# Performance work log

Hardware: AMD Instinct MI355X
Metric: run time of the kernel (lower is better)

The kernel has to match this reference:

```python
import jax, jax.numpy as jnp
import numpy as np

D_MODEL = 1024
NUM_HEADS = 16
WINDOW = 128
DEPTH = D_MODEL // NUM_HEADS


def setup_inputs() -> dict:
    key = jax.random.key(0)
    ks = jax.random.split(key, 9)
    B, S = 2, 2048
    scale = 1.0 / np.sqrt(D_MODEL)
    x = jax.random.normal(ks[0], (B, S, D_MODEL), dtype=jnp.float32)
    Wq = jax.random.normal(ks[1], (D_MODEL, D_MODEL), dtype=jnp.float32) * scale
    Wk = jax.random.normal(ks[2], (D_MODEL, D_MODEL), dtype=jnp.float32) * scale
    Wv = jax.random.normal(ks[3], (D_MODEL, D_MODEL), dtype=jnp.float32) * scale
    Wo = jax.random.normal(ks[4], (D_MODEL, D_MODEL), dtype=jnp.float32) * scale
    bq = jnp.zeros((D_MODEL,), jnp.float32)
    bk = jnp.zeros((D_MODEL,), jnp.float32)
    bv = jnp.zeros((D_MODEL,), jnp.float32)
    bo = jnp.zeros((D_MODEL,), jnp.float32)
    return {"x": x, "Wq": Wq, "bq": bq, "Wk": Wk, "bk": bk,
            "Wv": Wv, "bv": bv, "Wo": Wo, "bo": bo}


def _split_heads(t, B, S):
    # [B,S,D] -> [B,H,S,depth]
    return t.reshape(B, S, NUM_HEADS, DEPTH).transpose(0, 2, 1, 3)


def reference(x, Wq, bq, Wk, bk, Wv, bv, Wo, bo):
    B, S, _ = x.shape
    q = _split_heads(x @ Wq + bq, B, S)
    k = _split_heads(x @ Wk + bk, B, S)
    v = _split_heads(x @ Wv + bv, B, S)
    scores = jnp.einsum('bhqd,bhkd->bhqk', q, k) / jnp.sqrt(jnp.float32(DEPTH))
    idx = jnp.arange(S)
    # mask[i_row=j, i_col=i] per original: |i - j| <= window (symmetric)
    local = jnp.abs(idx[None, :] - idx[:, None]) <= WINDOW  # [S,S]
    scores = jnp.where(local[None, None], scores, jnp.float32(-1e9))
    attn = jax.nn.softmax(scores, axis=-1)
    out = jnp.einsum('bhqk,bhkd->bhqd', attn, v)
    concat = out.transpose(0, 2, 1, 3).reshape(B, S, D_MODEL)
    return concat @ Wo + bo
```

## Files before the change

kernel.cpp:

```cpp
#include <hip/hip_runtime.h>
#include <cstdint>
#include <cstddef>

typedef __attribute__((ext_vector_type(8))) short short8;
typedef __attribute__((ext_vector_type(4))) short short4v;
typedef __attribute__((ext_vector_type(4))) float f32x4;
typedef short8 bf16x8;

typedef __attribute__((address_space(1))) const unsigned GU;
typedef __attribute__((address_space(3))) unsigned LU;

__device__ __forceinline__ short f2bf(float f) {
  unsigned u = __builtin_bit_cast(unsigned, f);
  u += 0x7fffu + ((u >> 16) & 1u);
  return (short)(u >> 16);
}

__global__ __launch_bounds__(256) void k_cast_x(const float* __restrict__ x, short* __restrict__ xb) {
  size_t i = ((size_t)blockIdx.x * 256 + threadIdx.x) * 8;
  f32x4 a = *(const f32x4*)(x + i);
  f32x4 b = *(const f32x4*)(x + i + 4);
  short8 o;
#pragma unroll
  for (int j = 0; j < 4; ++j) { o[j] = f2bf(a[j]); o[4 + j] = f2bf(b[j]); }
  *(short8*)(xb + i) = o;
}

__global__ __launch_bounds__(256) void k_tw(const float* __restrict__ W0, const float* __restrict__ W1,
                                            const float* __restrict__ W2, const float* __restrict__ W3,
                                            short* __restrict__ WT) {
  __shared__ short T[64 * 72];
  int bid = blockIdx.x;
  int widx = bid >> 8;
  int t = bid & 255;
  int kr = (t >> 4) * 64, nc = (t & 15) * 64;
  const float* W = widx == 0 ? W0 : widx == 1 ? W1 : widx == 2 ? W2 : W3;
  short* out = WT + (size_t)widx * 1048576;
  int tid = threadIdx.x;
#pragma unroll
  for (int i = 0; i < 4; ++i) {
    int idx = tid + i * 256;
    int k = idx >> 4, n4 = (idx & 15) << 2;
    f32x4 v = *(const f32x4*)(W + (size_t)(kr + k) * 1024 + nc + n4);
#pragma unroll
    for (int j = 0; j < 4; ++j) T[(n4 + j) * 72 + k] = f2bf(v[j]);
  }
  __syncthreads();
#pragma unroll
  for (int i = 0; i < 2; ++i) {
    int idx = tid + i * 256;
    int n = idx >> 3, k8 = (idx & 7) << 3;
    *(short8*)(out + (size_t)(nc + n) * 1024 + kr + k8) = *(const short8*)&T[n * 72 + k8];
  }
}

__global__ __launch_bounds__(256) void k_tv(const short* __restrict__ v, short* __restrict__ vT) {
  __shared__ short T[64 * 72];
  int bid = blockIdx.x;
  int stile = bid & 31, h = (bid >> 5) & 15, b = bid >> 9;
  int s0 = stile * 64;
  int tid = threadIdx.x;
#pragma unroll
  for (int i = 0; i < 2; ++i) {
    int idx = tid + i * 256;
    int s = idx >> 3, d0 = (idx & 7) << 3;
    short8 vec = *(const short8*)(v + ((size_t)b * 2048 + s0 + s) * 1024 + h * 64 + d0);
#pragma unroll
    for (int j = 0; j < 8; ++j) T[(d0 + j) * 72 + s] = vec[j];
  }
  __syncthreads();
#pragma unroll
  for (int i = 0; i < 2; ++i) {
    int idx = tid + i * 256;
    int d = idx >> 3, s8 = (idx & 7) << 3;
    *(short8*)(vT + (((size_t)b * 16 + h) * 64 + d) * 2048 + s0 + s8) = *(const short8*)&T[d * 72 + s8];
  }
}

__global__ __launch_bounds__(512, 2) void k_gemm256(
    const short* __restrict__ A, const short* __restrict__ BT,
    const float* __restrict__ bias0, const float* __restrict__ bias1, const float* __restrict__ bias2,
    short* __restrict__ outb) {
  __shared__ short S[65536];
  const int tid = threadIdx.x;
  const int lane = tid & 63, w = tid >> 6;
  const int g = lane >> 4, qi = lane & 15;
  const int wm = w >> 2, wn = w & 3;
  int bid = blockIdx.x;
  int swz = (bid & 7) * 24 + (bid >> 3);
  const int tm = swz / 12, tn = swz % 12;
  const int m0 = tm * 256, n0 = tn * 256;
  const size_t K = 1024;
  const short* Ab = A + (size_t)m0 * K;
  const short* Bb = BT + (size_t)n0 * K;

  auto stage = [&](int roff, const short* gbase, int kt, int kh) {
    int k0 = kt * 64 + kh * 32;
#pragma unroll
    for (int i = 0; i < 2; ++i) {
      int c = tid + i * 512;
      int r = c >> 2;
      int csw = ((c & 3) ^ ((r >> 1) & 3)) << 3;
      __builtin_amdgcn_global_load_lds((GU*)(gbase + (size_t)r * K + k0 + csw),
                                       (LU*)(&S[roff + c * 8]), 16, 0, 0);
    }
  };
  auto lda = [&](int roff, int row) -> bf16x8 {
    return *(const bf16x8*)&S[roff + row * 32 + ((g ^ ((row >> 1) & 3)) << 3)];
  };

  f32x4 acc[8][4];
#pragma unroll
  for (int i = 0; i < 8; ++i)
#pragma unroll
    for (int j = 0; j < 4; ++j) acc[i][j] = (f32x4)(0.0f);

#define MF1(rh, mf, nf, av, bv) \
  acc[(rh)*4+(mf)][(nf)] = __builtin_amdgcn_mfma_f32_16x16x32_bf16(av, bv, acc[(rh)*4+(mf)][(nf)], 0, 0, 0)

#define GPH(buf, kh, rh, ...) do { \
    const int ra_ = (buf)*32768 + (kh)*8192; \
    const int rb_ = (buf)*32768 + 16384 + (kh)*8192; \
    const int ar_ = wm*128 + (rh)*64 + qi; \
    bf16x8 a0 = lda(ra_, ar_ + 0);  bf16x8 a1 = lda(ra_, ar_ + 16); \
    bf16x8 a2 = lda(ra_, ar_ + 32); bf16x8 a3 = lda(ra_, ar_ + 48); \
    const int br_ = wn*64 + qi; \
    bf16x8 b0 = lda(rb_, br_ + 0);  bf16x8 b1 = lda(rb_, br_ + 16); \
    bf16x8 b2 = lda(rb_, br_ + 32); bf16x8 b3 = lda(rb_, br_ + 48); \
    __VA_ARGS__; \
    __builtin_amdgcn_sched_barrier(0); \
    __builtin_amdgcn_s_barrier(); \
    asm volatile("s_waitcnt lgkmcnt(0)" ::: "memory"); \
    __builtin_amdgcn_sched_barrier(0); \
    __builtin_amdgcn_s_setprio(1); \
    MF1(rh,0,0,a0,b0); MF1(rh,0,1,a0,b1); MF1(rh,0,2,a0,b2); MF1(rh,0,3,a0,b3); \
    MF1(rh,1,0,a1,b0); MF1(rh,1,1,a1,b1); MF1(rh,1,2,a1,b2); MF1(rh,1,3,a1,b3); \
    MF1(rh,2,0,a2,b0); MF1(rh,2,1,a2,b1); MF1(rh,2,2,a2,b2); MF1(rh,2,3,a2,b3); \
    MF1(rh,3,0,a3,b0); MF1(rh,3,1,a3,b1); MF1(rh,3,2,a3,b2); MF1(rh,3,3,a3,b3); \
    __builtin_amdgcn_s_setprio(0); \
    __builtin_amdgcn_sched_barrier(0); \
  } while (0)

  stage(0,     Ab, 0, 0);
  stage(16384, Bb, 0, 0);
  stage(8192,  Ab, 0, 1);
  stage(24576, Bb, 0, 1);
  stage(32768, Ab, 1, 0);
  stage(49152, Bb, 1, 0);
  asm volatile("s_waitcnt vmcnt(4)" ::: "memory");
  __builtin_amdgcn_s_barrier();

  for (int j = 0; j < 8; ++j) {
    int t1 = 2 * j + 1;
    int t2 = 2 * j + 2; t2 = t2 < 15 ? t2 : 15;
    int t3 = 2 * j + 3; t3 = t3 < 15 ? t3 : 15;
    GPH(0, 0, 0, stage(40960, Ab, t1, 1));  __builtin_amdgcn_s_barrier();
    GPH(0, 0, 1, stage(57344, Bb, t1, 1));  __builtin_amdgcn_s_barrier();
    GPH(0, 1, 0, stage(0,     Ab, t2, 0));  __builtin_amdgcn_s_barrier();
    GPH(0, 1, 1, stage(16384, Bb, t2, 0));
      asm volatile("s_waitcnt vmcnt(4)" ::: "memory");
      __builtin_amdgcn_s_barrier();
    GPH(1, 0, 0, stage(8192,  Ab, t2, 1));  __builtin_amdgcn_s_barrier();
    GPH(1, 0, 1, stage(24576, Bb, t2, 1));  __builtin_amdgcn_s_barrier();
    GPH(1, 1, 0, stage(32768, Ab, t3, 0));  __builtin_amdgcn_s_barrier();
    GPH(1, 1, 1, stage(49152, Bb, t3, 0));
      asm volatile("s_waitcnt vmcnt(4)" ::: "memory");
      __builtin_amdgcn_s_barrier();
  }
#undef GPH
#undef MF1

  asm volatile("s_waitcnt vmcnt(0)" ::: "memory");
  __syncthreads();
  int sel = n0 >> 10;
  const float* bias = sel == 0 ? bias0 : (sel == 1 ? bias1 : bias2);
  size_t outoff = (size_t)sel * 4194304;
  int ncol0 = n0 & 1023;
  float bv[4];
#pragma unroll
  for (int nf = 0; nf < 4; ++nf) bv[nf] = bias[ncol0 + wn * 64 + nf * 16 + qi];
  short* Ep = S;
#pragma unroll
  for (int rh = 0; rh < 2; ++rh) {
    __syncthreads();
#pragma unroll
    for (int mf = 0; mf < 4; ++mf)
#pragma unroll
      for (int nf = 0; nf < 4; ++nf)
#pragma unroll
        for (int j = 0; j < 4; ++j)
          Ep[(wm * 64 + mf * 16 + g * 4 + j) * 264 + wn * 64 + nf * 16 + qi] =
              f2bf(acc[rh * 4 + mf][nf][j] + bv[nf]);
    __syncthreads();
#pragma unroll
    for (int i = 0; i < 8; ++i) {
      int idx = tid + i * 512;
      int r = idx >> 5, c8 = (idx & 31) << 3;
      int grow = m0 + (r >> 6) * 128 + rh * 64 + (r & 63);
      *(short8*)&outb[outoff + (size_t)grow * 1024 + ncol0 + c8] = *(const short8*)&Ep[r * 264 + c8];
    }
  }
}

__global__ __launch_bounds__(256, 2) void k_gemmO(
    const short* __restrict__ A, const short* __restrict__ BT,
    const float* __restrict__ bias0, float* __restrict__ outf) {
  __shared__ short Smem[16384];
  const int tid = threadIdx.x;
  const int lane = tid & 63, w = tid >> 6;
  const int g = lane >> 4, qi = lane & 15;
  const int wr = (w >> 1) * 64, wc = (w & 1) * 64;
  const int m0 = blockIdx.y * 128, n0 = blockIdx.x * 128;
  const size_t K = 1024;
  const short* Ab = A + (size_t)m0 * K;
  const short* Bb = BT + (size_t)n0 * K;

  auto stage = [&](int buf, int k0) {
    short* Asb = Smem + buf * 4096;
    short* Bsb = Smem + 8192 + buf * 4096;
#pragma unroll
    for (int i = 0; i < 2; ++i) {
      int cidx = tid + i * 256;
      int r = cidx >> 2;
      int csw = ((cidx & 3) ^ ((r >> 1) & 3)) << 3;
      __builtin_amdgcn_global_load_lds((GU*)(Ab + (size_t)r * K + k0 + csw),
                                       (LU*)(&Asb[cidx * 8]), 16, 0, 0);
      __builtin_amdgcn_global_load_lds((GU*)(Bb + (size_t)r * K + k0 + csw),
                                       (LU*)(&Bsb[cidx * 8]), 16, 0, 0);
    }
  };

  f32x4 acc[4][4];
#pragma unroll
  for (int i = 0; i < 4; ++i)
#pragma unroll
    for (int j = 0; j < 4; ++j) acc[i][j] = (f32x4)(0.0f);

  stage(0, 0);
  __syncthreads();
  for (int kt = 0; kt < 32; ++kt) {
    int cur = kt & 1;
    if (kt < 31) stage(cur ^ 1, (kt + 1) * 32);
    const short* Asb = Smem + cur * 4096;
    const short* Bsb = Smem + 8192 + cur * 4096;
    bf16x8 a[4], b[4];
#pragma unroll
    for (int mf = 0; mf < 4; ++mf) {
      int R = wr + mf * 16 + qi;
      a[mf] = *(const bf16x8*)&Asb[R * 32 + ((g ^ ((R >> 1) & 3)) << 3)];
    }
#pragma unroll
    for (int nf = 0; nf < 4; ++nf) {
      int R = wc + nf * 16 + qi;
      b[nf] = *(const bf16x8*)&Bsb[R * 32 + ((g ^ ((R >> 1) & 3)) << 3)];
    }
#pragma unroll
    for (int mf = 0; mf < 4; ++mf)
#pragma unroll
      for (int nf = 0; nf < 4; ++nf)
        acc[mf][nf] = __builtin_amdgcn_mfma_f32_16x16x32_bf16(a[mf], b[nf], acc[mf][nf], 0, 0, 0);
    __syncthreads();
  }

  float* Ft = (float*)Smem;
  float bv[4];
#pragma unroll
  for (int nf = 0; nf < 4; ++nf) bv[nf] = bias0[n0 + wc + nf * 16 + qi];
#pragma unroll
  for (int mf = 0; mf < 4; ++mf) {
    __syncthreads();
#pragma unroll
    for (int nf = 0; nf < 4; ++nf)
#pragma unroll
      for (int j = 0; j < 4; ++j)
        Ft[((w >> 1) * 16 + g * 4 + j) * 136 + wc + nf * 16 + qi] = acc[mf][nf][j] + bv[nf];
    __syncthreads();
#pragma unroll
    for (int i = 0; i < 4; ++i) {
      int idx = tid + i * 256;
      int r = idx >> 5, c4 = (idx & 31) << 2;
      int row = m0 + ((r >> 4) << 6) + mf * 16 + (r & 15);
      *(f32x4*)&outf[(size_t)row * 1024 + n0 + c4] = *(const f32x4*)&Ft[r * 136 + c4];
    }
  }
}

__global__ __launch_bounds__(256, 2) void k_attn(const short* __restrict__ qg_,
                                                 const short* __restrict__ kg_,
                                                 const short* __restrict__ vT,
                                                 short* __restrict__ outp) {
  __shared__ short Qs[64 * 72];
  __shared__ short Ks[64 * 72];
  __shared__ short Vs[64 * 72];
  __shared__ short Ps[4][16 * 72];
  int bid = blockIdx.x;
  int qt = bid & 31, h = (bid >> 5) & 15, b = bid >> 9;
  int q0 = qt * 64;
  int tid = threadIdx.x, lane = tid & 63, w = tid >> 6;
  int g = lane >> 4, qi = lane & 15;

  const short* qsrc = qg_ + ((size_t)b * 2048 + q0) * 1024 + h * 64;
#pragma unroll
  for (int i = 0; i < 2; ++i) {
    int idx = tid + i * 256;
    int r = idx >> 3, c = (idx & 7) << 3;
    *(short8*)&Qs[r * 72 + c] = *(const short8*)&qsrc[(size_t)r * 1024 + c];
  }

  float m = -1e30f, l = 0.f;
  f32x4 oacc[4];
#pragma unroll
  for (int i = 0; i < 4; ++i) oacc[i] = (f32x4)(0.0f);
  int qglob = q0 + w * 16 + qi;

  for (int cc = 0; cc < 5; ++cc) {
    int kb0 = q0 - 128 + cc * 64;
    if (kb0 < 0 || kb0 >= 2048) continue;
    __syncthreads();
    const short* ksrc = kg_ + ((size_t)b * 2048 + kb0) * 1024 + h * 64;
    const short* vsrc = vT + ((size_t)(b * 16 + h)) * 64 * 2048 + kb0;
#pragma unroll
    for (int i = 0; i < 2; ++i) {
      int idx = tid + i * 256;
      int r = idx >> 3, c = (idx & 7) << 3;
      *(short8*)&Ks[r * 72 + c] = *(const short8*)&ksrc[(size_t)r * 1024 + c];
      *(short8*)&Vs[r * 72 + c] = *(const short8*)&vsrc[(size_t)r * 2048 + c];
    }
    __syncthreads();

    f32x4 st[4];
#pragma unroll
    for (int i = 0; i < 4; ++i) st[i] = (f32x4)(0.0f);
#pragma unroll
    for (int ds = 0; ds < 2; ++ds) {
      bf16x8 qf = *(const bf16x8*)&Qs[(w * 16 + qi) * 72 + ds * 32 + g * 8];
#pragma unroll
      for (int mf = 0; mf < 4; ++mf) {
        bf16x8 kf = *(const bf16x8*)&Ks[(mf * 16 + qi) * 72 + ds * 32 + g * 8];
        st[mf] = __builtin_amdgcn_mfma_f32_16x16x32_bf16(kf, qf, st[mf], 0, 0, 0);
      }
    }

    float pv[16];
    float pm = -1e30f;
#pragma unroll
    for (int mf = 0; mf < 4; ++mf)
#pragma unroll
      for (int j = 0; j < 4; ++j) {
        int kcol = kb0 + mf * 16 + g * 4 + j;
        float s = st[mf][j] * 0.125f;
        int d = kcol - qglob;
        bool valid = (d >= -128) && (d <= 128);
        s = valid ? s : -1e30f;
        pv[mf * 4 + j] = s;
        pm = fmaxf(pm, s);
      }
    pm = fmaxf(pm, __shfl_xor(pm, 16));
    pm = fmaxf(pm, __shfl_xor(pm, 32));
    float mnew = fmaxf(m, pm);
    float scale = __expf(m - mnew);
    float ls = 0.f;
#pragma unroll
    for (int e = 0; e < 16; ++e) {
      float p = pv[e] > -1e29f ? __expf(pv[e] - mnew) : 0.f;
      pv[e] = p;
      ls += p;
    }
    ls += __shfl_xor(ls, 16);
    ls += __shfl_xor(ls, 32);
    l = l * scale + ls;
    m = mnew;
#pragma unroll
    for (int mf = 0; mf < 4; ++mf) oacc[mf] *= scale;

#pragma unroll
    for (int f = 0; f < 4; ++f) {
      short4v pk;
#pragma unroll
      for (int j = 0; j < 4; ++j) pk[j] = f2bf(pv[f * 4 + j]);
      *(short4v*)&Ps[w][qi * 72 + f * 16 + g * 4] = pk;
    }

#pragma unroll
    for (int ks = 0; ks < 2; ++ks) {
      bf16x8 pf = *(const bf16x8*)&Ps[w][qi * 72 + ks * 32 + g * 8];
#pragma unroll
      for (int mf = 0; mf < 4; ++mf) {
        bf16x8 vf = *(const bf16x8*)&Vs[(mf * 16 + qi) * 72 + ks * 32 + g * 8];
        oacc[mf] = __builtin_amdgcn_mfma_f32_16x16x32_bf16(vf, pf, oacc[mf], 0, 0, 0);
      }
    }
  }

  __syncthreads();
  short* Os = Ks;
  float inv = 1.f / l;
#pragma unroll
  for (int mf = 0; mf < 4; ++mf) {
    short4v pk;
#pragma unroll
    for (int j = 0; j < 4; ++j) pk[j] = f2bf(oacc[mf][j] * inv);
    *(short4v*)&Os[(w * 16 + qi) * 72 + mf * 16 + g * 4] = pk;
  }
  __syncthreads();
  short* dst = outp + ((size_t)b * 2048 + q0) * 1024 + h * 64;
  int r = tid >> 2, c16 = (tid & 3) << 4;
  *(short8*)&dst[(size_t)r * 1024 + c16] = *(const short8*)&Os[r * 72 + c16];
  *(short8*)&dst[(size_t)r * 1024 + c16 + 8] = *(const short8*)&Os[r * 72 + c16 + 8];
}

extern "C" void kernel_launch(void* const* d_in, const int* in_sizes, int n_in,
                              void* d_out, int out_size, void* d_ws, size_t ws_size,
                              hipStream_t stream) {
  const float* x  = (const float*)d_in[0];
  const float* Wq = (const float*)d_in[1];
  const float* bq = (const float*)d_in[2];
  const float* Wk = (const float*)d_in[3];
  const float* bk = (const float*)d_in[4];
  const float* Wv = (const float*)d_in[5];
  const float* bv = (const float*)d_in[6];
  const float* Wo = (const float*)d_in[7];
  const float* bo = (const float*)d_in[8];

  short* ws = (short*)d_ws;
  short* xb       = ws;
  short* qkv      = ws + 4194304;
  short* vbuf     = qkv + 2 * 4194304;
  short* vT       = ws;
  short* attn_out = vbuf;
  short* WT       = ws + 4 * 4194304;

  k_cast_x<<<2048, 256, 0, stream>>>(x, xb);
  k_tw<<<1024, 256, 0, stream>>>(Wq, Wk, Wv, Wo, WT);
  k_gemm256<<<192, 512, 0, stream>>>(xb, WT, bq, bk, bv, qkv);
  k_tv<<<1024, 256, 0, stream>>>(vbuf, vT);
  k_attn<<<1024, 256, 0, stream>>>(qkv, qkv + 4194304, vT, attn_out);
  {
    dim3 grid(8, 32);
    k_gemmO<<<grid, 256, 0, stream>>>(attn_out, WT + 3 * 1048576, bo, (float*)d_out);
  }
}
```

Baseline: 92.98 us.

## Switch QKV GEMM from 16x16x32 to 32x32x16 MFMA tiles

Reworks the fused QKV projection GEMM so each wave computes its 128x64 tile with 32x32x16 bf16 MFMA instructions instead of 16x16x32. This cuts the number of LDS fragment loads per MFMA and restructures the per-phase schedule, with partial lgkmcnt waits so half the MFMAs can start while the rest of the LDS reads finish. The epilogue is rewritten for the 32x32 accumulator layout. Larger accumulators and a different LDS access pattern may change register pressure and bank conflicts.

```diff
diff --git a/kernel.cpp b/kernel.cpp
--- a/kernel.cpp
+++ b/kernel.cpp
@@ -5,6 +5,7 @@
 typedef __attribute__((ext_vector_type(8))) short short8;
 typedef __attribute__((ext_vector_type(4))) short short4v;
 typedef __attribute__((ext_vector_type(4))) float f32x4;
+typedef __attribute__((ext_vector_type(16))) float f32x16;
 typedef short8 bf16x8;
 
 typedef __attribute__((address_space(1))) const unsigned GU;
@@ -84,7 +85,7 @@
   __shared__ short S[65536];
   const int tid = threadIdx.x;
   const int lane = tid & 63, w = tid >> 6;
-  const int g = lane >> 4, qi = lane & 15;
+  const int l31 = lane & 31, hi = lane >> 5;
   const int wm = w >> 2, wn = w & 3;
   int bid = blockIdx.x;
   int swz = (bid & 7) * 24 + (bid >> 3);
@@ -105,38 +106,58 @@
                                        (LU*)(&S[roff + c * 8]), 16, 0, 0);
     }
   };
-  auto lda = [&](int roff, int row) -> bf16x8 {
-    return *(const bf16x8*)&S[roff + row * 32 + ((g ^ ((row >> 1) & 3)) << 3)];
+  auto lda = [&](int roff, int row, int s) -> bf16x8 {
+    int c = (s * 2 + hi) ^ ((row >> 1) & 3);
+    return *(const bf16x8*)&S[roff + row * 32 + c * 8];
   };
 
-  f32x4 acc[8][4];
-#pragma unroll
-  for (int i = 0; i < 8; ++i)
-#pragma unroll
-    for (int j = 0; j < 4; ++j) acc[i][j] = (f32x4)(0.0f);
-
-#define MF1(rh, mf, nf, av, bv) \
-  acc[(rh)*4+(mf)][(nf)] = __builtin_amdgcn_mfma_f32_16x16x32_bf16(av, bv, acc[(rh)*4+(mf)][(nf)], 0, 0, 0)
-
-#define GPH(buf, kh, rh, ...) do { \
-    const int ra_ = (buf)*32768 + (kh)*8192; \
-    const int rb_ = (buf)*32768 + 16384 + (kh)*8192; \
-    const int ar_ = wm*128 + (rh)*64 + qi; \
-    bf16x8 a0 = lda(ra_, ar_ + 0);  bf16x8 a1 = lda(ra_, ar_ + 16); \
-    bf16x8 a2 = lda(ra_, ar_ + 32); bf16x8 a3 = lda(ra_, ar_ + 48); \
-    const int br_ = wn*64 + qi; \
-    bf16x8 b0 = lda(rb_, br_ + 0);  bf16x8 b1 = lda(rb_, br_ + 16); \
-    bf16x8 b2 = lda(rb_, br_ + 32); bf16x8 b3 = lda(rb_, br_ + 48); \
-    __VA_ARGS__; \
+  f32x16 acc[4][2];
+#pragma unroll
+  for (int i = 0; i < 4; ++i)
+#pragma unroll
+    for (int j = 0; j < 2; ++j) acc[i][j] = (f32x16)(0.0f);
+
+#define MFA(mi, ni, av, bv) \
+  acc[mi][ni] = __builtin_amdgcn_mfma_f32_32x32x16_bf16(av, bv, acc[mi][ni], 0, 0, 0)
+#define VMC4 asm volatile("s_waitcnt vmcnt(4)" ::: "memory")
+#define NOVM (void)0
+
+#define GPP(buf, kh, STG0, STG1, VM1) do { \
+    const int rA_ = (buf)*32768 + (kh)*8192; \
+    const int rB_ = (buf)*32768 + 16384 + (kh)*8192; \
+    const int ar_ = wm*128 + l31; \
+    const int br_ = wn*64 + l31; \
+    bf16x8 a00 = lda(rA_, ar_,      0); bf16x8 a10 = lda(rA_, ar_ + 32, 0); \
+    bf16x8 b00 = lda(rB_, br_,      0); bf16x8 b10 = lda(rB_, br_ + 32, 0); \
+    bf16x8 a01 = lda(rA_, ar_,      1); bf16x8 a11 = lda(rA_, ar_ + 32, 1); \
+    bf16x8 b01 = lda(rB_, br_,      1); bf16x8 b11 = lda(rB_, br_ + 32, 1); \
+    STG0; \
     __builtin_amdgcn_sched_barrier(0); \
     __builtin_amdgcn_s_barrier(); \
+    asm volatile("s_waitcnt lgkmcnt(4)" ::: "memory"); \
+    __builtin_amdgcn_sched_barrier(0); \
+    __builtin_amdgcn_s_setprio(1); \
+    MFA(0,0,a00,b00); MFA(0,1,a00,b10); MFA(1,0,a10,b00); MFA(1,1,a10,b10); \
+    __builtin_amdgcn_sched_barrier(0); \
     asm volatile("s_waitcnt lgkmcnt(0)" ::: "memory"); \
     __builtin_amdgcn_sched_barrier(0); \
+    MFA(0,0,a01,b01); MFA(0,1,a01,b11); MFA(1,0,a11,b01); MFA(1,1,a11,b11); \
+    __builtin_amdgcn_s_setprio(0); \
+    __builtin_amdgcn_sched_barrier(0); \
+    bf16x8 c00 = lda(rA_, ar_ + 64, 0); bf16x8 c10 = lda(rA_, ar_ + 96, 0); \
+    bf16x8 c01 = lda(rA_, ar_ + 64, 1); bf16x8 c11 = lda(rA_, ar_ + 96, 1); \
+    STG1; \
+    VM1; \
+    __builtin_amdgcn_sched_barrier(0); \
+    __builtin_amdgcn_s_barrier(); \
+    asm volatile("s_waitcnt lgkmcnt(2)" ::: "memory"); \
+    __builtin_amdgcn_sched_barrier(0); \
     __builtin_amdgcn_s_setprio(1); \
-    MF1(rh,0,0,a0,b0); MF1(rh,0,1,a0,b1); MF1(rh,0,2,a0,b2); MF1(rh,0,3,a0,b3); \
-    MF1(rh,1,0,a1,b0); MF1(rh,1,1,a1,b1); MF1(rh,1,2,a1,b2); MF1(rh,1,3,a1,b3); \
-    MF1(rh,2,0,a2,b0); MF1(rh,2,1,a2,b1); MF1(rh,2,2,a2,b2); MF1(rh,2,3,a2,b3); \
-    MF1(rh,3,0,a3,b0); MF1(rh,3,1,a3,b1); MF1(rh,3,2,a3,b2); MF1(rh,3,3,a3,b3); \
+    MFA(2,0,c00,b00); MFA(2,1,c00,b10); MFA(3,0,c10,b00); MFA(3,1,c10,b10); \
+    __builtin_amdgcn_sched_barrier(0); \
+    asm volatile("s_waitcnt lgkmcnt(0)" ::: "memory"); \
+    __builtin_amdgcn_sched_barrier(0); \
+    MFA(2,0,c01,b01); MFA(2,1,c01,b11); MFA(3,0,c11,b01); MFA(3,1,c11,b11); \
     __builtin_amdgcn_s_setprio(0); \
     __builtin_amdgcn_sched_barrier(0); \
   } while (0)
@@ -154,21 +175,13 @@
     int t1 = 2 * j + 1;
     int t2 = 2 * j + 2; t2 = t2 < 15 ? t2 : 15;
     int t3 = 2 * j + 3; t3 = t3 < 15 ? t3 : 15;
-    GPH(0, 0, 0, stage(40960, Ab, t1, 1));  __builtin_amdgcn_s_barrier();
-    GPH(0, 0, 1, stage(57344, Bb, t1, 1));  __builtin_amdgcn_s_barrier();
-    GPH(0, 1, 0, stage(0,     Ab, t2, 0));  __builtin_amdgcn_s_barrier();
-    GPH(0, 1, 1, stage(16384, Bb, t2, 0));
-      asm volatile("s_waitcnt vmcnt(4)" ::: "memory");
-      __builtin_amdgcn_s_barrier();
-    GPH(1, 0, 0, stage(8192,  Ab, t2, 1));  __builtin_amdgcn_s_barrier();
-    GPH(1, 0, 1, stage(24576, Bb, t2, 1));  __builtin_amdgcn_s_barrier();
-    GPH(1, 1, 0, stage(32768, Ab, t3, 0));  __builtin_amdgcn_s_barrier();
-    GPH(1, 1, 1, stage(49152, Bb, t3, 0));
-      asm volatile("s_waitcnt vmcnt(4)" ::: "memory");
-      __builtin_amdgcn_s_barrier();
-  }
-#undef GPH
-#undef MF1
+    GPP(0, 0, stage(40960, Ab, t1, 1), stage(57344, Bb, t1, 1), NOVM);
+    GPP(0, 1, stage(0,     Ab, t2, 0), stage(16384, Bb, t2, 0), VMC4);
+    GPP(1, 0, stage(8192,  Ab, t2, 1), stage(24576, Bb, t2, 1), NOVM);
+    GPP(1, 1, stage(32768, Ab, t3, 0), stage(49152, Bb, t3, 0), VMC4);
+  }
+#undef GPP
+#undef MFA
 
   asm volatile("s_waitcnt vmcnt(0)" ::: "memory");
   __syncthreads();
@@ -176,27 +189,31 @@
   const float* bias = sel == 0 ? bias0 : (sel == 1 ? bias1 : bias2);
   size_t outoff = (size_t)sel * 4194304;
   int ncol0 = n0 & 1023;
-  float bv[4];
-#pragma unroll
-  for (int nf = 0; nf < 4; ++nf) bv[nf] = bias[ncol0 + wn * 64 + nf * 16 + qi];
+  float bv[2];
+#pragma unroll
+  for (int ni = 0; ni < 2; ++ni) bv[ni] = bias[ncol0 + wn * 64 + ni * 32 + l31];
   short* Ep = S;
 #pragma unroll
-  for (int rh = 0; rh < 2; ++rh) {
-    __syncthreads();
-#pragma unroll
-    for (int mf = 0; mf < 4; ++mf)
-#pragma unroll
-      for (int nf = 0; nf < 4; ++nf)
-#pragma unroll
-        for (int j = 0; j < 4; ++j)
-          Ep[(wm * 64 + mf * 16 + g * 4 + j) * 264 + wn * 64 + nf * 16 + qi] =
-              f2bf(acc[rh * 4 + mf][nf][j] + bv[nf]);
+  for (int p = 0; p < 2; ++p) {
+    __syncthreads();
+#pragma unroll
+    for (int mi2 = 0; mi2 < 2; ++mi2)
+#pragma unroll
+      for (int ni = 0; ni < 2; ++ni)
+#pragma unroll
+        for (int rq = 0; rq < 4; ++rq)
+#pragma unroll
+          for (int jj = 0; jj < 4; ++jj) {
+            int rif = jj + 4 * hi + 8 * rq;
+            Ep[(wm * 64 + mi2 * 32 + rif) * 264 + wn * 64 + ni * 32 + l31] =
+                f2bf(acc[p * 2 + mi2][ni][rq * 4 + jj] + bv[ni]);
+          }
     __syncthreads();
 #pragma unroll
     for (int i = 0; i < 8; ++i) {
       int idx = tid + i * 512;
       int r = idx >> 5, c8 = (idx & 31) << 3;
-      int grow = m0 + (r >> 6) * 128 + rh * 64 + (r & 63);
+      int grow = m0 + (r >> 6) * 128 + p * 64 + (r & 63);
       *(short8*)&outb[outoff + (size_t)grow * 1024 + ncol0 + c8] = *(const short8*)&Ep[r * 264 + c8];
     }
   }
```

Result: no change. 92.61 us (-0.4%).

## Restructure QKV GEMM main loop into full-K64 stages with interleaved LDS reads

Applied to the files above, without the earlier changes.

Reworks the 256x256 QKV projection GEMM so each pipeline stage loads a full 64-wide K slice per 128-row half, with a new 8-way XOR swizzle. The hand-scheduled loop interleaves partial lgkmcnt waits with MFMA groups and issues the next tiles' global-to-LDS loads between compute chunks. This is meant to cut barriers per K step and overlap LDS reads with MFMA work. Warps now own contiguous 128-row strips, so the epilogue is reorganised to write one strip per pass. The cost is higher register pressure from double-buffered fragments and a more fragile wait-count schedule.

```diff
diff --git a/kernel.cpp b/kernel.cpp
--- a/kernel.cpp
+++ b/kernel.cpp
@@ -94,19 +94,18 @@
   const short* Ab = A + (size_t)m0 * K;
   const short* Bb = BT + (size_t)n0 * K;
 
-  auto stage = [&](int roff, const short* gbase, int kt, int kh) {
-    int k0 = kt * 64 + kh * 32;
+  auto stage = [&](int roff, const short* gbase, int kt) {
 #pragma unroll
     for (int i = 0; i < 2; ++i) {
-      int c = tid + i * 512;
-      int r = c >> 2;
-      int csw = ((c & 3) ^ ((r >> 1) & 3)) << 3;
-      __builtin_amdgcn_global_load_lds((GU*)(gbase + (size_t)r * K + k0 + csw),
-                                       (LU*)(&S[roff + c * 8]), 16, 0, 0);
+      int cc = tid + i * 512;
+      int r = cc >> 3;
+      int js = ((cc & 7) ^ (r & 7)) << 3;
+      __builtin_amdgcn_global_load_lds((GU*)(gbase + (size_t)r * K + kt * 64 + js),
+                                       (LU*)(&S[roff + cc * 8]), 16, 0, 0);
     }
   };
-  auto lda = [&](int roff, int row) -> bf16x8 {
-    return *(const bf16x8*)&S[roff + row * 32 + ((g ^ ((row >> 1) & 3)) << 3)];
+  auto lda = [&](int roff, int row, int kk) -> bf16x8 {
+    return *(const bf16x8*)&S[roff + row * 64 + (((kk * 4 + g) ^ (row & 7)) << 3)];
   };
 
   f32x4 acc[8][4];
@@ -115,60 +114,88 @@
 #pragma unroll
     for (int j = 0; j < 4; ++j) acc[i][j] = (f32x4)(0.0f);
 
-#define MF1(rh, mf, nf, av, bv) \
-  acc[(rh)*4+(mf)][(nf)] = __builtin_amdgcn_mfma_f32_16x16x32_bf16(av, bv, acc[(rh)*4+(mf)][(nf)], 0, 0, 0)
-
-#define GPH(buf, kh, rh, ...) do { \
-    const int ra_ = (buf)*32768 + (kh)*8192; \
-    const int rb_ = (buf)*32768 + 16384 + (kh)*8192; \
-    const int ar_ = wm*128 + (rh)*64 + qi; \
-    bf16x8 a0 = lda(ra_, ar_ + 0);  bf16x8 a1 = lda(ra_, ar_ + 16); \
-    bf16x8 a2 = lda(ra_, ar_ + 32); bf16x8 a3 = lda(ra_, ar_ + 48); \
-    const int br_ = wn*64 + qi; \
-    bf16x8 b0 = lda(rb_, br_ + 0);  bf16x8 b1 = lda(rb_, br_ + 16); \
-    bf16x8 b2 = lda(rb_, br_ + 32); bf16x8 b3 = lda(rb_, br_ + 48); \
-    __VA_ARGS__; \
-    __builtin_amdgcn_sched_barrier(0); \
-    __builtin_amdgcn_s_barrier(); \
-    asm volatile("s_waitcnt lgkmcnt(0)" ::: "memory"); \
-    __builtin_amdgcn_sched_barrier(0); \
-    __builtin_amdgcn_s_setprio(1); \
-    MF1(rh,0,0,a0,b0); MF1(rh,0,1,a0,b1); MF1(rh,0,2,a0,b2); MF1(rh,0,3,a0,b3); \
-    MF1(rh,1,0,a1,b0); MF1(rh,1,1,a1,b1); MF1(rh,1,2,a1,b2); MF1(rh,1,3,a1,b3); \
-    MF1(rh,2,0,a2,b0); MF1(rh,2,1,a2,b1); MF1(rh,2,2,a2,b2); MF1(rh,2,3,a2,b3); \
-    MF1(rh,3,0,a3,b0); MF1(rh,3,1,a3,b1); MF1(rh,3,2,a3,b2); MF1(rh,3,3,a3,b3); \
-    __builtin_amdgcn_s_setprio(0); \
-    __builtin_amdgcn_sched_barrier(0); \
-  } while (0)
-
-  stage(0,     Ab, 0, 0);
-  stage(16384, Bb, 0, 0);
-  stage(8192,  Ab, 0, 1);
-  stage(24576, Bb, 0, 1);
-  stage(32768, Ab, 1, 0);
-  stage(49152, Bb, 1, 0);
+#define MFA(mi, ni, av, bv) \
+  acc[mi][ni] = __builtin_amdgcn_mfma_f32_16x16x32_bf16(av, bv, acc[mi][ni], 0, 0, 0)
+#define SB __builtin_amdgcn_sched_barrier(0)
+
+  stage(0,     Ab,          0);
+  stage(8192,  Ab + 131072, 0);
+  stage(16384, Bb,          0);
+  stage(24576, Bb + 131072, 0);
+  stage(49152, Bb,          1);
+  stage(57344, Bb + 131072, 1);
   asm volatile("s_waitcnt vmcnt(4)" ::: "memory");
   __builtin_amdgcn_s_barrier();
 
-  for (int j = 0; j < 8; ++j) {
-    int t1 = 2 * j + 1;
-    int t2 = 2 * j + 2; t2 = t2 < 15 ? t2 : 15;
-    int t3 = 2 * j + 3; t3 = t3 < 15 ? t3 : 15;
-    GPH(0, 0, 0, stage(40960, Ab, t1, 1));  __builtin_amdgcn_s_barrier();
-    GPH(0, 0, 1, stage(57344, Bb, t1, 1));  __builtin_amdgcn_s_barrier();
-    GPH(0, 1, 0, stage(0,     Ab, t2, 0));  __builtin_amdgcn_s_barrier();
-    GPH(0, 1, 1, stage(16384, Bb, t2, 0));
-      asm volatile("s_waitcnt vmcnt(4)" ::: "memory");
-      __builtin_amdgcn_s_barrier();
-    GPH(1, 0, 0, stage(8192,  Ab, t2, 1));  __builtin_amdgcn_s_barrier();
-    GPH(1, 0, 1, stage(24576, Bb, t2, 1));  __builtin_amdgcn_s_barrier();
-    GPH(1, 1, 0, stage(32768, Ab, t3, 0));  __builtin_amdgcn_s_barrier();
-    GPH(1, 1, 1, stage(49152, Bb, t3, 0));
-      asm volatile("s_waitcnt vmcnt(4)" ::: "memory");
-      __builtin_amdgcn_s_barrier();
-  }
-#undef GPH
-#undef MF1
+  for (int t = 0; t < 16; ++t) {
+    const int b = t & 1, nb = b ^ 1;
+    const int rA = b * 32768 + wm * 8192;
+    const int rB = b * 32768 + 16384 + (wn >> 1) * 8192;
+    const int brow = (wn & 1) * 64;
+    const int t1 = t + 1 < 15 ? t + 1 : 15;
+    const int t2 = t + 2 < 15 ? t + 2 : 15;
+    bf16x8 aA[8], aB[4], cA[8], cB[4];
+
+    stage(nb * 32768, Ab, t1);
+#pragma unroll
+    for (int mf = 0; mf < 4; ++mf) aA[mf] = lda(rA, mf * 16 + qi, 0);
+#pragma unroll
+    for (int nf = 0; nf < 4; ++nf) aB[nf] = lda(rB, brow + nf * 16 + qi, 0);
+    SB;
+#pragma unroll
+    for (int mf = 4; mf < 8; ++mf) aA[mf] = lda(rA, mf * 16 + qi, 0);
+    asm volatile("s_waitcnt lgkmcnt(4)" ::: "memory");
+    SB;
+    __builtin_amdgcn_s_setprio(1);
+#pragma unroll
+    for (int mf = 0; mf < 4; ++mf)
+#pragma unroll
+      for (int nf = 0; nf < 4; ++nf) MFA(mf, nf, aA[mf], aB[nf]);
+    __builtin_amdgcn_s_setprio(0);
+    SB;
+    stage(nb * 32768 + 8192, Ab + 131072, t1);
+#pragma unroll
+    for (int mf = 0; mf < 4; ++mf) cA[mf] = lda(rA, mf * 16 + qi, 1);
+#pragma unroll
+    for (int nf = 0; nf < 4; ++nf) cB[nf] = lda(rB, brow + nf * 16 + qi, 1);
+    SB;
+#pragma unroll
+    for (int mf = 4; mf < 8; ++mf) cA[mf] = lda(rA, mf * 16 + qi, 1);
+    asm volatile("s_waitcnt lgkmcnt(12)" ::: "memory");
+    SB;
+    __builtin_amdgcn_s_setprio(1);
+#pragma unroll
+    for (int mf = 4; mf < 8; ++mf)
+#pragma unroll
+      for (int nf = 0; nf < 4; ++nf) MFA(mf, nf, aA[mf], aB[nf]);
+    __builtin_amdgcn_s_setprio(0);
+    SB;
+    __builtin_amdgcn_s_barrier();
+    stage(b * 32768 + 16384, Bb, t2);
+    asm volatile("s_waitcnt lgkmcnt(4)" ::: "memory");
+    SB;
+    __builtin_amdgcn_s_setprio(1);
+#pragma unroll
+    for (int mf = 0; mf < 4; ++mf)
+#pragma unroll
+      for (int nf = 0; nf < 4; ++nf) MFA(mf, nf, cA[mf], cB[nf]);
+    __builtin_amdgcn_s_setprio(0);
+    SB;
+    stage(b * 32768 + 24576, Bb + 131072, t2);
+    asm volatile("s_waitcnt vmcnt(4)" ::: "memory");
+    asm volatile("s_waitcnt lgkmcnt(0)" ::: "memory");
+    SB;
+    __builtin_amdgcn_s_setprio(1);
+#pragma unroll
+    for (int mf = 4; mf < 8; ++mf)
+#pragma unroll
+      for (int nf = 0; nf < 4; ++nf) MFA(mf, nf, cA[mf], cB[nf]);
+    __builtin_amdgcn_s_setprio(0);
+    SB;
+    __builtin_amdgcn_s_barrier();
+  }
+#undef MFA
+#undef SB
 
   asm volatile("s_waitcnt vmcnt(0)" ::: "memory");
   __syncthreads();
@@ -181,22 +208,24 @@
   for (int nf = 0; nf < 4; ++nf) bv[nf] = bias[ncol0 + wn * 64 + nf * 16 + qi];
   short* Ep = S;
 #pragma unroll
-  for (int rh = 0; rh < 2; ++rh) {
-    __syncthreads();
-#pragma unroll
-    for (int mf = 0; mf < 4; ++mf)
-#pragma unroll
-      for (int nf = 0; nf < 4; ++nf)
-#pragma unroll
-        for (int j = 0; j < 4; ++j)
-          Ep[(wm * 64 + mf * 16 + g * 4 + j) * 264 + wn * 64 + nf * 16 + qi] =
-              f2bf(acc[rh * 4 + mf][nf][j] + bv[nf]);
+  for (int p = 0; p < 2; ++p) {
+    __syncthreads();
+    if (wm == p) {
+#pragma unroll
+      for (int mf = 0; mf < 8; ++mf)
+#pragma unroll
+        for (int nf = 0; nf < 4; ++nf)
+#pragma unroll
+          for (int j = 0; j < 4; ++j)
+            Ep[(mf * 16 + g * 4 + j) * 264 + wn * 64 + nf * 16 + qi] =
+                f2bf(acc[mf][nf][j] + bv[nf]);
+    }
     __syncthreads();
 #pragma unroll
     for (int i = 0; i < 8; ++i) {
       int idx = tid + i * 512;
       int r = idx >> 5, c8 = (idx & 31) << 3;
-      int grow = m0 + (r >> 6) * 128 + rh * 64 + (r & 63);
+      int grow = m0 + p * 128 + r;
       *(short8*)&outb[outoff + (size_t)grow * 1024 + ncol0 + c8] = *(const short8*)&Ep[r * 264 + c8];
     }
   }
```

Measured after the change: 90.00 us. 1.03x faster.
